# Kernel tuning notes

Hardware: AMD Instinct MI355X
Metric: run time of the kernel (lower is better)

Reference implementation:

```python
import jax, jax.numpy as jnp
import numpy as np

H = 64       # hidden size hard-coded in the module
NH = 4       # n_heads
S = 500      # stock_num
D = 10       # num_day
T = 40       # num_text (news per day)
FP = 3       # price features
FT = 512     # text embedding dim


def gru_scan(x, Wih, Whh, bih, bhh):
    """Single-sequence GRU (torch gate convention). x: (T, F) -> hidden states (T, H)."""
    gi = x @ Wih + bih  # (T, 3H) precompute input gates outside the scan

    def step(h, g):
        gh = h @ Whh + bhh
        r = jax.nn.sigmoid(g[:H] + gh[:H])
        z = jax.nn.sigmoid(g[H:2 * H] + gh[H:2 * H])
        n = jnp.tanh(g[2 * H:] + r * gh[2 * H:])
        h_new = (1.0 - z) * n + z * h
        return h_new, h_new

    h0 = jnp.zeros((H,), x.dtype)
    _, hs = jax.lax.scan(step, h0, gi)
    return hs


def attn_pool(hs, W, v):
    """Additive attention pooling over time. hs: (T, H) -> (H,)."""
    scores = jnp.tanh(hs @ W) @ v          # (T,)
    alpha = jax.nn.softmax(scores)
    return alpha @ hs


def _gru_params(key, fin, scale=0.08):
    k1, k2, k3, k4 = jax.random.split(key, 4)
    return (jax.random.normal(k1, (S, fin, 3 * H)) * scale,
            jax.random.normal(k2, (S, H, 3 * H)) * scale,
            jax.random.normal(k3, (S, 3 * H)) * scale,
            jax.random.normal(k4, (S, 3 * H)) * scale)


def _attn_params(key, scale=0.08):
    k1, k2 = jax.random.split(key)
    return (jax.random.normal(k1, (S, H, H)) * scale,
            jax.random.normal(k2, (S, H)) * scale)


def setup_inputs() -> dict:
    key = jax.random.key(0)
    ks = jax.random.split(key, 20)
    inp = {}
    inp['text_input'] = jax.random.normal(ks[0], (S, D, T, FT), dtype=jnp.float32)
    inp['price_input'] = jax.random.normal(ks[1], (S, D, FP), dtype=jnp.float32)
    inp['label'] = jax.random.randint(ks[2], (S,), 0, 2)
    inp['adj'] = jnp.ones((S, S), dtype=jnp.float32)
    inp['train'] = 0
    # per-stock stacked parameters
    (inp['Wih_p'], inp['Whh_p'], inp['bih_p'], inp['bhh_p']) = _gru_params(ks[3], FP)
    (inp['Wa_p'], inp['va_p']) = _attn_params(ks[4])
    (inp['Wih_t'], inp['Whh_t'], inp['bih_t'], inp['bhh_t']) = _gru_params(ks[5], FT)
    (inp['Wa_t'], inp['va_t']) = _attn_params(ks[6])
    (inp['Wih_s'], inp['Whh_s'], inp['bih_s'], inp['bhh_s']) = _gru_params(ks[7], H)
    (inp['Wa_s'], inp['va_s']) = _attn_params(ks[8])
    inp['Wb'] = jax.random.normal(ks[9], (S, H, H, H)) * 0.05   # Bilinear weight (out,in1,in2)
    inp['bb'] = jax.random.normal(ks[10], (S, H)) * 0.05
    inp['Wbl'] = jax.random.normal(ks[11], (S, H, 2)) * 0.08
    inp['bbl'] = jax.random.normal(ks[12], (S, 2)) * 0.08
    # shared cross-stock self-attention projections and final fc
    inp['Wq'] = jax.random.normal(ks[13], (H, H)) * 0.08
    inp['bq'] = jax.random.normal(ks[14], (H,)) * 0.08
    inp['Wk'] = jax.random.normal(ks[15], (H, H)) * 0.08
    inp['bk'] = jax.random.normal(ks[16], (H,)) * 0.08
    inp['Wf'] = jax.random.normal(ks[17], (H, 2)) * 0.08
    inp['bf'] = jax.random.normal(ks[18], (2,)) * 0.08
    return inp


def _forward(text_input, price_input, label,
             Wih_p, Whh_p, bih_p, bhh_p, Wa_p, va_p,
             Wih_t, Whh_t, bih_t, bhh_t, Wa_t, va_t,
             Wih_s, Whh_s, bih_s, bhh_s, Wa_s, va_s,
             Wb, bb, Wbl, bbl, Wq, bq, Wk, bk, Wf, bf):
    # ---- per-stock price encoder: GRU over days + attention pooling ----
    def enc_price(x, a, b, c, d, W, v):
        return attn_pool(gru_scan(x, a, b, c, d), W, v)
    x_price = jax.vmap(enc_price)(price_input, Wih_p, Whh_p, bih_p, bhh_p, Wa_p, va_p)  # (S, H)

    # ---- per-stock, per-day text encoder ----
    def enc_text_stock(xdays, a, b, c, d, W, v):
        return jax.vmap(lambda x: attn_pool(gru_scan(x, a, b, c, d), W, v))(xdays)  # (D, H)
    news = jax.vmap(enc_text_stock)(text_input, Wih_t, Whh_t, bih_t, bhh_t, Wa_t, va_t)  # (S, D, H)

    # ---- per-stock sequence encoder over days ----
    text_vec = jax.vmap(enc_price)(news, Wih_s, Whh_s, bih_s, bhh_s, Wa_s, va_s)  # (S, H)

    # ---- bilinear fusion: tanh(Bilinear(text, price)) ----
    combined = jnp.tanh(jnp.einsum('si,skij,sj->sk', text_vec, Wb, x_price) + bb)  # (S, H)

    # ---- per-stock blending head ----
    out_1 = jnp.tanh(jnp.einsum('si,sik->sk', combined, Wbl) + bbl)  # (S, 2)

    # ---- cross-stock multi-head self-attention (q,k projected, v identity) ----
    dh = H // NH
    q = (combined @ Wq + bq).reshape(S, NH, dh)
    k = (combined @ Wk + bk).reshape(S, NH, dh)
    v = combined.reshape(S, NH, dh)
    scores = jnp.einsum('shd,thd->hst', q, k) / (dh ** 0.5)
    attn = jax.nn.softmax(scores, axis=-1)
    attn_out = jnp.einsum('hst,thd->shd', attn, v).reshape(S, H)

    x = jax.nn.elu(attn_out @ Wf + bf)  # (S, 2)
    output = jax.nn.softmax(x + out_1, axis=1)
    # faithful to the original: CrossEntropyLoss applied to already-softmaxed output
    logp = jax.nn.log_softmax(output, axis=1)
    loss = -jnp.mean(logp[jnp.arange(S), label])
    return loss, output


def reference(text_input, price_input, label, adj, train,
              Wih_p, Whh_p, bih_p, bhh_p, Wa_p, va_p,
              Wih_t, Whh_t, bih_t, bhh_t, Wa_t, va_t,
              Wih_s, Whh_s, bih_s, bhh_s, Wa_s, va_s,
              Wb, bb, Wbl, bbl, Wq, bq, Wk, bk, Wf, bf):
    return _forward(text_input, price_input, label,
                    Wih_p, Whh_p, bih_p, bhh_p, Wa_p, va_p,
                    Wih_t, Whh_t, bih_t, bhh_t, Wa_t, va_t,
                    Wih_s, Whh_s, bih_s, bhh_s, Wa_s, va_s,
                    Wb, bb, Wbl, bbl, Wq, bq, Wk, bk, Wf, bf)
```

## Files before the change

kernel.cpp:

```cpp
#include <hip/hip_runtime.h>

#define Sn 500
#define Dn 10
#define Tn 40
#define FPn 3
#define FTn 512
#define Hn 64
#define G3 192
#define NHn 4

typedef __attribute__((ext_vector_type(8))) short bf8_t;
typedef __attribute__((ext_vector_type(4))) float f4_t;

__device__ __forceinline__ unsigned short f2bf(float f) {
    union { float f; unsigned int u; } v; v.f = f;
    unsigned int r = v.u + 0x7fffu + ((v.u >> 16) & 1u);
    return (unsigned short)(r >> 16);
}
__device__ __forceinline__ float bflo(unsigned int u) {
    union { unsigned int u; float f; } v; v.u = u << 16; return v.f;
}
__device__ __forceinline__ float bfhi(unsigned int u) {
    union { unsigned int u; float f; } v; v.u = u & 0xffff0000u; return v.f;
}
__device__ __forceinline__ unsigned int cvtpk(float lo, float hi) {
    unsigned int r;
    asm("v_cvt_pk_bf16_f32 %0, %1, %2" : "=v"(r) : "v"(lo), "v"(hi));
    return r;
}
__device__ __forceinline__ float sigmoidf_(float x) { return 1.f / (1.f + __expf(-x)); }
__device__ __forceinline__ float tanhf_(float x) {
    x = fminf(15.f, fmaxf(-15.f, x));
    float e = __expf(2.f * x);
    return (e - 1.f) / (e + 1.f);
}
__device__ __forceinline__ float dot8(uint4 wv, f4_t hA, f4_t hB) {
    return bflo(wv.x) * hA[0] + bfhi(wv.x) * hA[1]
         + bflo(wv.y) * hA[2] + bfhi(wv.y) * hA[3]
         + bflo(wv.z) * hB[0] + bfhi(wv.z) * hB[1]
         + bflo(wv.w) * hB[2] + bfhi(wv.w) * hB[3];
}
union bfu { bf8_t v; unsigned int u[4]; };

__global__ __launch_bounds__(256) void prep_fused(
    const float* __restrict__ Wih, unsigned short* __restrict__ wt,
    const float* __restrict__ price, const float* __restrict__ Wih_p,
    const float* __restrict__ Whh_p, const float* __restrict__ bih_p,
    const float* __restrict__ bhh_p, const float* __restrict__ Wa_p,
    const float* __restrict__ va_p, float* __restrict__ xprice)
{
    __shared__ float tile[64][65];
    __shared__ __align__(16) unsigned char smp[33160];

    const int bid = blockIdx.x, tid = threadIdx.x;

    if (bid < 12000) {
        const int s = bid / 24, tlo = bid % 24;
        const int kt = tlo / 3, ct = tlo % 3;
        const int k0 = kt * 64, c0 = ct * 64;

        const int c = tid & 63, r0 = tid >> 6;
        const float* src = Wih + ((size_t)s * FTn + k0) * G3 + c0 + c;
        #pragma unroll
        for (int i = 0; i < 16; ++i) {
            int r = i * 4 + r0;
            tile[c][r] = src[(size_t)r * G3];
        }
        __syncthreads();

        const int cl = tid >> 5, k2 = (tid & 31) * 2;
        unsigned int* wo = (unsigned int*)wt;
        const int kc = (k0 >> 3) + (k2 >> 3), e2 = (k2 & 7) >> 1;
        #pragma unroll
        for (int p = 0; p < 8; ++p) {
            int col = cl + p * 8;
            wo[(size_t)s * 49152 + ((size_t)kc * G3 + c0 + col) * 4 + e2] =
                cvtpk(tile[col][k2], tile[col][k2 + 1]);
        }
        return;
    }

    const int s = bid - 12000;
    if (tid >= 64) return;
    const int l = tid;
    unsigned char* whh2 = smp;
    unsigned char* wa2 = smp + 24576;
    float* hbuf = (float*)(smp + 32768);
    float* priceL = (float*)(smp + 33040);

    {
        const float* W3 = Whh_p + (size_t)s * Hn * G3;
        for (int r = 0; r < 192; ++r) {
            int e = l + r * 64, i = e / G3, j = e - i * G3;
            *(unsigned short*)(whh2 + j * 128 + ((2 * i) ^ ((j & 7) << 4))) = f2bf(W3[e]);
        }
        const float* A3 = Wa_p + (size_t)s * Hn * Hn;
        for (int r = 0; r < 64; ++r) {
            int e = l + r * 64, i = e >> 6, k = e & 63;
            *(unsigned short*)(wa2 + k * 128 + ((2 * i) ^ ((k & 7) << 4))) = f2bf(A3[e]);
        }
        if (l < 30) priceL[l] = price[(size_t)s * 30 + l];
        hbuf[l] = 0.f;
        if (l < 4) hbuf[64 + l] = 0.f;
    }
    __builtin_amdgcn_wave_barrier();
    {
        float wp[3][3];
        #pragma unroll
        for (int i = 0; i < 3; ++i)
            #pragma unroll
            for (int g = 0; g < 3; ++g)
                wp[i][g] = Wih_p[(size_t)s * 3 * G3 + i * G3 + g * 64 + l];
        const float bi0 = bih_p[(size_t)s * G3 + l];
        const float bi1 = bih_p[(size_t)s * G3 + 64 + l];
        const float bi2 = bih_p[(size_t)s * G3 + 128 + l];
        const float bh0 = bhh_p[(size_t)s * G3 + l];
        const float bh1 = bhh_p[(size_t)s * G3 + 64 + l];
        const float bh2 = bhh_p[(size_t)s * G3 + 128 + l];
        const float vak = va_p[(size_t)s * Hn + l];
        const int swl = (l & 7) << 4;
        float h3 = 0.f, m3 = -1e30f, den3 = 0.f, av3 = 0.f;
        for (int t = 0; t < Dn; ++t) {
            float x0 = priceL[t * 3], x1 = priceL[t * 3 + 1], x2 = priceL[t * 3 + 2];
            float gg0 = bi0 + x0 * wp[0][0] + x1 * wp[1][0] + x2 * wp[2][0];
            float gg1 = bi1 + x0 * wp[0][1] + x1 * wp[1][1] + x2 * wp[2][1];
            float gg2 = bi2 + x0 * wp[0][2] + x1 * wp[1][2] + x2 * wp[2][2];
            float gh0 = bh0, gh1 = bh1, gh2 = bh2;
            #pragma unroll
            for (int ic = 0; ic < 8; ++ic) {
                const int off = (ic * 16) ^ swl;
                f4_t hA = *(const f4_t*)&hbuf[ic * 8];
                f4_t hB = *(const f4_t*)&hbuf[ic * 8 + 4];
                uint4 w0 = *(const uint4*)(whh2 + l * 128 + off);
                uint4 w1 = *(const uint4*)(whh2 + (l + 64) * 128 + off);
                uint4 w2 = *(const uint4*)(whh2 + (l + 128) * 128 + off);
                gh0 += dot8(w0, hA, hB); gh1 += dot8(w1, hA, hB); gh2 += dot8(w2, hA, hB);
            }
            float r = sigmoidf_(gg0 + gh0);
            float z = sigmoidf_(gg1 + gh1);
            float n = tanhf_(gg2 + r * gh2);
            h3 = (1.f - z) * n + z * h3;
            __builtin_amdgcn_wave_barrier();
            hbuf[l] = h3;
            __builtin_amdgcn_wave_barrier();
            float sk = 0.f;
            #pragma unroll
            for (int ic = 0; ic < 8; ++ic) {
                const int off = (ic * 16) ^ swl;
                uint4 wv = *(const uint4*)(wa2 + l * 128 + off);
                f4_t hA = *(const f4_t*)&hbuf[ic * 8];
                f4_t hB = *(const f4_t*)&hbuf[ic * 8 + 4];
                sk += dot8(wv, hA, hB);
            }
            float term = tanhf_(sk) * vak;
            #pragma unroll
            for (int off = 32; off; off >>= 1) term += __shfl_xor(term, off);
            float mn = fmaxf(m3, term);
            float s0 = __expf(m3 - mn);
            float p = __expf(term - mn);
            den3 = den3 * s0 + p;
            av3 = av3 * s0 + p * h3;
            m3 = mn;
        }
        xprice[(size_t)s * Hn + l] = av3 / den3;
    }
}

__global__ __launch_bounds__(256) void main_fused(
    const float* __restrict__ text, const unsigned short* __restrict__ wt,
    const float* __restrict__ bih, float* __restrict__ gi2,
    const float* __restrict__ Wb, const float* __restrict__ xprice,
    float* __restrict__ u)
{
    __shared__ __align__(16) unsigned char sm[20480];

    const int id = blockIdx.x;
    const int grp = id / 9, sub = id - grp * 9;
    const int tid = threadIdx.x, w = tid >> 6, l = tid & 63;

    if (sub < 5) {
        const int s = grp, fi = sub;
        const int lr = l & 15, kg = l >> 4;
        unsigned short* Ab0 = (unsigned short*)sm;
        unsigned short* Ab1 = Ab0 + 5120;

        const float* xbase = text + ((size_t)s * 400 + fi * 80) * FTn;
        const unsigned short* wtb = wt + (size_t)s * 98304 + (size_t)(w * 48 + lr) * 8;

        const int c0 = tid, c1 = tid + 256, c2 = tid + 512;

        f4_t acc[5][3];
        #pragma unroll
        for (int a = 0; a < 5; a++)
            #pragma unroll
            for (int b = 0; b < 3; b++) acc[a][b] = (f4_t){0.f, 0.f, 0.f, 0.f};

        f4_t pa[3], pb[3];
        auto aload = [&](int kk) {
            #pragma unroll
            for (int q = 0; q < 3; ++q) {
                int c = tid + q * 256;
                if (q < 2 || tid < 128) {
                    int row = c >> 3, slot = c & 7;
                    const float* p = xbase + (size_t)row * FTn + kk * 64 + slot * 8;
                    pa[q] = *(const f4_t*)p; pb[q] = *(const f4_t*)(p + 4);
                }
            }
        };
        auto awrite = [&](unsigned short* buf) {
            #pragma unroll
            for (int q = 0; q < 3; ++q) {
                int c = tid + q * 256;
                if (q < 2 || tid < 128) {
                    int row = c >> 3, slot = c & 7;
                    uint4 uu = { cvtpk(pa[q][0], pa[q][1]), cvtpk(pa[q][2], pa[q][3]),
                                 cvtpk(pb[q][0], pb[q][1]), cvtpk(pb[q][2], pb[q][3]) };
                    *(uint4*)(buf + row * 64 + ((slot ^ (row & 7)) * 8)) = uu;
                }
            }
        };
        auto bload = [&](int kk, int ks, int nc) -> bf8_t {
            return *(const bf8_t*)(wtb + (size_t)((kk * 8 + ks * 4 + kg) * G3 + nc * 16) * 8);
        };
        auto afrag = [&](const unsigned short* buf, int mt, int ks) -> bf8_t {
            int row = mt * 16 + lr;
            int slot = (ks * 4 + kg) ^ (row & 7);
            return *(const bf8_t*)(buf + row * 64 + slot * 8);
        };

        bf8_t bc[2][3], bn[2][3];
        aload(0);
        #pragma unroll
        for (int ks = 0; ks < 2; ++ks)
            #pragma unroll
            for (int nc = 0; nc < 3; ++nc) bc[ks][nc] = bload(0, ks, nc);
        awrite(Ab0);
        __syncthreads();

        for (int kk = 0; kk < 8; ++kk) {
            unsigned short* cur = (kk & 1) ? Ab1 : Ab0;
            unsigned short* nxt = (kk & 1) ? Ab0 : Ab1;
            if (kk < 7) {
                aload(kk + 1);
                #pragma unroll
                for (int ks = 0; ks < 2; ++ks)
                    #pragma unroll
                    for (int nc = 0; nc < 3; ++nc) bn[ks][nc] = bload(kk + 1, ks, nc);
            }
            #pragma unroll
            for (int ks = 0; ks < 2; ++ks)
                #pragma unroll
                for (int mt = 0; mt < 5; ++mt) {
                    bf8_t af = afrag(cur, mt, ks);
                    acc[mt][0] = __builtin_amdgcn_mfma_f32_16x16x32_bf16(af, bc[ks][0], acc[mt][0], 0, 0, 0);
                    acc[mt][1] = __builtin_amdgcn_mfma_f32_16x16x32_bf16(af, bc[ks][1], acc[mt][1], 0, 0, 0);
                    acc[mt][2] = __builtin_amdgcn_mfma_f32_16x16x32_bf16(af, bc[ks][2], acc[mt][2], 0, 0, 0);
                }
            if (kk < 7) awrite(nxt);
            __syncthreads();
            #pragma unroll
            for (int ks = 0; ks < 2; ++ks)
                #pragma unroll
                for (int nc = 0; nc < 3; ++nc) bc[ks][nc] = bn[ks][nc];
        }

        const float* bihs = bih + (size_t)s * G3 + w * 48 + lr;
        #pragma unroll
        for (int nc = 0; nc < 3; ++nc) {
            const int col = w * 48 + nc * 16 + lr;
            const float bv = bihs[nc * 16];
            #pragma unroll
            for (int mt = 0; mt < 5; ++mt)
                #pragma unroll
                for (int rg = 0; rg < 4; ++rg) {
                    int r = mt * 16 + kg * 4 + rg;
                    int hi = (r >= 40);
                    int day = fi * 2 + hi;
                    int t = r - hi * 40;
                    gi2[((size_t)(s * 40 + t) * 10 + day) * 192 + col] = acc[mt][nc][rg] + bv;
                }
        }
    } else {
        const int s = grp, kq = sub - 5;
        float* uT = (float*)sm;
        const int j4 = (l & 15) * 4;
        f4_t xq = *(const f4_t*)&xprice[s * Hn + j4];

        const float* Wbs = Wb + (size_t)s * Hn * Hn * Hn;
        for (int g = 0; g < 64; ++g) {
            int P = kq * 1024 + w * 256 + g * 4 + (l >> 4);
            f4_t wv = *(const f4_t*)&Wbs[(size_t)P * Hn + j4];
            float dp = wv[0] * xq[0] + wv[1] * xq[1] + wv[2] * xq[2] + wv[3] * xq[3];
            dp += __shfl_xor(dp, 8);
            dp += __shfl_xor(dp, 4);
            dp += __shfl_xor(dp, 2);
            dp += __shfl_xor(dp, 1);
            if ((l & 15) == 0) { int k = P >> 6, i = P & 63; uT[i * 17 + (k - kq * 16)] = dp; }
        }
        __syncthreads();
        #pragma unroll
        for (int r = 0; r < 4; ++r) {
            int flat = tid + r * 256;
            int kr = flat >> 6, i = flat & 63;
            u[((size_t)s * 64 + kq * 16 + kr) * 64 + i] = uT[i * 17 + kr];
        }
    }
}

__global__ __launch_bounds__(64, 1) void gru_text_f(
    const float* __restrict__ gi2, const float* __restrict__ Whh,
    const float* __restrict__ bhh, const float* __restrict__ Wa,
    const float* __restrict__ va, float* __restrict__ news)
{
    __shared__ __align__(16) float hrow[16 * 68];
    __shared__ __align__(16) unsigned char waT[Hn * 128];

    const int s = blockIdx.x, l = threadIdx.x;
    const int lr = l & 15, lg = l >> 4;

    const float* Whhs = Whh + (size_t)s * Hn * G3;
    bfu bwhh[2][12];
    #pragma unroll
    for (int ks = 0; ks < 2; ++ks)
        #pragma unroll
        for (int nt = 0; nt < 12; ++nt) {
            const float* p = Whhs + (size_t)(ks * 32 + lg * 8) * G3 + nt * 16 + lr;
            float b0 = p[0], b1 = p[G3], b2 = p[2 * G3], b3 = p[3 * G3];
            float b4 = p[4 * G3], b5 = p[5 * G3], b6 = p[6 * G3], b7 = p[7 * G3];
            bwhh[ks][nt].u[0] = cvtpk(b0, b1); bwhh[ks][nt].u[1] = cvtpk(b2, b3);
            bwhh[ks][nt].u[2] = cvtpk(b4, b5); bwhh[ks][nt].u[3] = cvtpk(b6, b7);
        }
    float bhh_l[12];
    #pragma unroll
    for (int nt = 0; nt < 12; ++nt) bhh_l[nt] = bhh[(size_t)s * G3 + nt * 16 + lr];
    float va_l[4];
    #pragma unroll
    for (int nt = 0; nt < 4; ++nt) va_l[nt] = va[(size_t)s * Hn + nt * 16 + lr];

    {
        const float* Was = Wa + (size_t)s * Hn * Hn;
        for (int r = 0; r < 64; ++r) {
            int e = l + r * 64, i = e >> 6, k = e & 63;
            *(unsigned short*)(waT + k * 128 + ((2 * i) ^ ((k & 7) << 4))) = f2bf(Was[e]);
        }
        #pragma unroll
        for (int r = 0; r < 17; ++r) hrow[l + r * 64] = 0.f;
    }
    __builtin_amdgcn_wave_barrier();

    int dayoff[4];
    #pragma unroll
    for (int rr = 0; rr < 4; ++rr) {
        int d = lg * 4 + rr; if (d > 9) d = 9;
        dayoff[rr] = d * 192 + lr;
    }
    const float* gbase = gi2 + (size_t)s * 40 * 1920;

    float val[48], valn[48];
    #pragma unroll
    for (int j = 0; j < 48; ++j) val[j] = gbase[dayoff[j & 3] + (j >> 2) * 16];

    bf8_t a0f, a1f;
    {   bfu z0; z0.u[0] = 0; z0.u[1] = 0; z0.u[2] = 0; z0.u[3] = 0; a0f = z0.v; a1f = z0.v; }

    float h[4][4], accv[4][4], den[4], m[4];
    #pragma unroll
    for (int nt = 0; nt < 4; ++nt)
        #pragma unroll
        for (int rr = 0; rr < 4; ++rr) { h[nt][rr] = 0.f; accv[nt][rr] = 0.f; }
    #pragma unroll
    for (int rr = 0; rr < 4; ++rr) { den[rr] = 0.f; m[rr] = -1e30f; }

    for (int t = 0; t < Tn; ++t) {
        f4_t acc[12];
        #pragma unroll
        for (int nt = 0; nt < 12; ++nt)
            acc[nt] = (f4_t){bhh_l[nt], bhh_l[nt], bhh_l[nt], bhh_l[nt]};
        __builtin_amdgcn_s_setprio(1);
        #pragma unroll
        for (int nt = 0; nt < 12; ++nt) {
            acc[nt] = __builtin_amdgcn_mfma_f32_16x16x32_bf16(a0f, bwhh[0][nt].v, acc[nt], 0, 0, 0);
            acc[nt] = __builtin_amdgcn_mfma_f32_16x16x32_bf16(a1f, bwhh[1][nt].v, acc[nt], 0, 0, 0);
        }
        __builtin_amdgcn_s_setprio(0);
        {
            const int tn = (t < Tn - 1) ? t + 1 : t;
            const float* gb = gbase + (size_t)tn * 1920;
            #pragma unroll
            for (int j = 0; j < 48; ++j) valn[j] = gb[dayoff[j & 3] + (j >> 2) * 16];
        }
        #pragma unroll
        for (int nt = 0; nt < 4; ++nt)
            #pragma unroll
            for (int rr = 0; rr < 4; ++rr) {
                float r = sigmoidf_(val[nt * 4 + rr] + acc[nt][rr]);
                float z = sigmoidf_(val[(nt + 4) * 4 + rr] + acc[nt + 4][rr]);
                float n = tanhf_(val[(nt + 8) * 4 + rr] + r * acc[nt + 8][rr]);
                h[nt][rr] = (1.f - z) * n + z * h[nt][rr];
            }
        __builtin_amdgcn_wave_barrier();
        #pragma unroll
        for (int rr = 0; rr < 4; ++rr) {
            int day = lg * 4 + rr;
            if (day < Dn) {
                #pragma unroll
                for (int nt = 0; nt < 4; ++nt) hrow[day * 68 + nt * 16 + lr] = h[nt][rr];
            }
        }
        __builtin_amdgcn_wave_barrier();
        {
            const float* hp = hrow + lr * 68 + lg * 8;
            f4_t x0 = *(const f4_t*)hp,        x1 = *(const f4_t*)(hp + 4);
            f4_t y0 = *(const f4_t*)(hp + 32), y1 = *(const f4_t*)(hp + 36);
            bfu t0, t1;
            t0.u[0] = cvtpk(x0[0], x0[1]); t0.u[1] = cvtpk(x0[2], x0[3]);
            t0.u[2] = cvtpk(x1[0], x1[1]); t0.u[3] = cvtpk(x1[2], x1[3]);
            t1.u[0] = cvtpk(y0[0], y0[1]); t1.u[1] = cvtpk(y0[2], y0[3]);
            t1.u[2] = cvtpk(y1[0], y1[1]); t1.u[3] = cvtpk(y1[2], y1[3]);
            a0f = t0.v; a1f = t1.v;
        }
        f4_t sc[4];
        #pragma unroll
        for (int nt = 0; nt < 4; ++nt) sc[nt] = (f4_t){0.f, 0.f, 0.f, 0.f};
        __builtin_amdgcn_s_setprio(1);
        #pragma unroll
        for (int ks = 0; ks < 2; ++ks) {
            bf8_t av = ks ? a1f : a0f;
            #pragma unroll
            for (int nt = 0; nt < 4; ++nt) {
                bf8_t bwv = *(const bf8_t*)(waT + (nt * 16 + lr) * 128
                                            + ((ks * 64 + lg * 16) ^ ((lr & 7) << 4)));
                sc[nt] = __builtin_amdgcn_mfma_f32_16x16x32_bf16(av, bwv, sc[nt], 0, 0, 0);
            }
        }
        __builtin_amdgcn_s_setprio(0);
        float pr[4];
        #pragma unroll
        for (int rr = 0; rr < 4; ++rr) {
            pr[rr] = tanhf_(sc[0][rr]) * va_l[0] + tanhf_(sc[1][rr]) * va_l[1]
                   + tanhf_(sc[2][rr]) * va_l[2] + tanhf_(sc[3][rr]) * va_l[3];
            pr[rr] += __shfl_xor(pr[rr], 1);
            pr[rr] += __shfl_xor(pr[rr], 2);
            pr[rr] += __shfl_xor(pr[rr], 4);
            pr[rr] += __shfl_xor(pr[rr], 8);
        }
        #pragma unroll
        for (int rr = 0; rr < 4; ++rr) {
            float mn = fmaxf(m[rr], pr[rr]);
            float s0 = __expf(m[rr] - mn);
            float p = __expf(pr[rr] - mn);
            den[rr] = den[rr] * s0 + p;
            #pragma unroll
            for (int nt = 0; nt < 4; ++nt)
                accv[nt][rr] = accv[nt][rr] * s0 + p * h[nt][rr];
            m[rr] = mn;
        }
        #pragma unroll
        for (int j = 0; j < 48; ++j) val[j] = valn[j];
    }
    #pragma unroll
    for (int rr = 0; rr < 4; ++rr) {
        int day = lg * 4 + rr;
        if (day < Dn) {
            float inv = 1.f / den[rr];
            #pragma unroll
            for (int nt = 0; nt < 4; ++nt)
                news[((size_t)s * Dn + day) * Hn + nt * 16 + lr] = accv[nt][rr] * inv;
        }
    }
}

__global__ __launch_bounds__(64, 1) void day_finish(
    const float* __restrict__ news,
    const float* __restrict__ Wih_s, const float* __restrict__ Whh_s,
    const float* __restrict__ bih_s, const float* __restrict__ bhh_s,
    const float* __restrict__ Wa_s, const float* __restrict__ va_s,
    const float* __restrict__ u, const float* __restrict__ bb,
    const float* __restrict__ Wq, const float* __restrict__ bq,
    const float* __restrict__ Wk, const float* __restrict__ bk,
    const float* __restrict__ Wbl, const float* __restrict__ bbl,
    float* __restrict__ combined, float* __restrict__ qg,
    float* __restrict__ kg, float* __restrict__ out1)
{
    __shared__ __align__(16) unsigned char sm[60928];
    unsigned char* whh2 = sm;
    unsigned char* wih2 = sm + 24576;
    unsigned char* wa2 = sm + 49152;
    float* newsL = (float*)(sm + 57600);
    float* hbuf  = (float*)(sm + 60320);

    const int s = blockIdx.x, l = threadIdx.x;
    float tvv;

    {
        const float* W2 = Whh_s + (size_t)s * Hn * G3;
        const float* X2 = Wih_s + (size_t)s * Hn * G3;
        for (int r = 0; r < 192; ++r) {
            int e = l + r * 64, i = e / G3, j = e - i * G3;
            int off = j * 128 + ((2 * i) ^ ((j & 7) << 4));
            *(unsigned short*)(whh2 + off) = f2bf(W2[e]);
            *(unsigned short*)(wih2 + off) = f2bf(X2[e]);
        }
        const float* A2 = Wa_s + (size_t)s * Hn * Hn;
        for (int r = 0; r < 64; ++r) {
            int e = l + r * 64, i = e >> 6, k = e & 63;
            *(unsigned short*)(wa2 + k * 128 + ((2 * i) ^ ((k & 7) << 4))) = f2bf(A2[e]);
        }
        #pragma unroll
        for (int d = 0; d < Dn; ++d) newsL[d * 68 + l] = news[((size_t)s * Dn + d) * Hn + l];
        hbuf[l] = 0.f;
        if (l < 4) hbuf[64 + l] = 0.f;
    }
    __builtin_amdgcn_wave_barrier();
    {
        const float bi0 = bih_s[(size_t)s * G3 + l];
        const float bi1 = bih_s[(size_t)s * G3 + 64 + l];
        const float bi2 = bih_s[(size_t)s * G3 + 128 + l];
        const float bh0 = bhh_s[(size_t)s * G3 + l];
        const float bh1 = bhh_s[(size_t)s * G3 + 64 + l];
        const float bh2 = bhh_s[(size_t)s * G3 + 128 + l];
        const float vak = va_s[(size_t)s * Hn + l];
        const int swl = (l & 7) << 4;
        float h2 = 0.f, m2 = -1e30f, den2 = 0.f, av2 = 0.f;
        for (int t = 0; t < Dn; ++t) {
            float gh0 = bh0, gh1 = bh1, gh2 = bh2;
            float gg0 = bi0, gg1 = bi1, gg2 = bi2;
            #pragma unroll
            for (int ic = 0; ic < 8; ++ic) {
                const int off = (ic * 16) ^ swl;
                f4_t hA = *(const f4_t*)&hbuf[ic * 8];
                f4_t hB = *(const f4_t*)&hbuf[ic * 8 + 4];
                f4_t nA = *(const f4_t*)&newsL[t * 68 + ic * 8];
                f4_t nB = *(const f4_t*)&newsL[t * 68 + ic * 8 + 4];
                uint4 w0 = *(const uint4*)(whh2 + l * 128 + off);
                uint4 w1 = *(const uint4*)(whh2 + (l + 64) * 128 + off);
                uint4 w2 = *(const uint4*)(whh2 + (l + 128) * 128 + off);
                uint4 x0 = *(const uint4*)(wih2 + l * 128 + off);
                uint4 x1 = *(const uint4*)(wih2 + (l + 64) * 128 + off);
                uint4 x2 = *(const uint4*)(wih2 + (l + 128) * 128 + off);
                gh0 += dot8(w0, hA, hB); gh1 += dot8(w1, hA, hB); gh2 += dot8(w2, hA, hB);
                gg0 += dot8(x0, nA, nB); gg1 += dot8(x1, nA, nB); gg2 += dot8(x2, nA, nB);
            }
            float r = sigmoidf_(gg0 + gh0);
            float z = sigmoidf_(gg1 + gh1);
            float n = tanhf_(gg2 + r * gh2);
            h2 = (1.f - z) * n + z * h2;
            __builtin_amdgcn_wave_barrier();
            hbuf[l] = h2;
            __builtin_amdgcn_wave_barrier();
            float sk = 0.f;
            #pragma unroll
            for (int ic = 0; ic < 8; ++ic) {
                const int off = (ic * 16) ^ swl;
                uint4 wv = *(const uint4*)(wa2 + l * 128 + off);
                f4_t hA = *(const f4_t*)&hbuf[ic * 8];
                f4_t hB = *(const f4_t*)&hbuf[ic * 8 + 4];
                sk += dot8(wv, hA, hB);
            }
            float term = tanhf_(sk) * vak;
            #pragma unroll
            for (int off = 32; off; off >>= 1) term += __shfl_xor(term, off);
            float mn = fmaxf(m2, term);
            float s0 = __expf(m2 - mn);
            float p = __expf(term - mn);
            den2 = den2 * s0 + p;
            av2 = av2 * s0 + p * h2;
            m2 = mn;
        }
        tvv = av2 / den2;
    }
    __builtin_amdgcn_wave_barrier();

    float* uL = (float*)sm;
    float* tvL = (float*)(sm + 16640);
    float* cl  = (float*)(sm + 16960);
    tvL[l] = tvv;
    const float* ub = u + (size_t)s * 4096;
    #pragma unroll 8
    for (int i = 0; i < 64; ++i) uL[i * 65 + l] = ub[i * 64 + l];
    __builtin_amdgcn_wave_barrier();
    {
        float a = bb[s * Hn + l];
        #pragma unroll 8
        for (int i = 0; i < 64; ++i) a += tvL[i] * uL[l * 65 + i];
        float c = tanhf_(a);
        cl[l] = c;
        combined[s * Hn + l] = c;
    }
    __builtin_amdgcn_wave_barrier();
    {
        float aq = bq[l], ak = bk[l];
        for (int i = 0; i < Hn; i++) {
            float ci = cl[i];
            aq += ci * Wq[i * Hn + l];
            ak += ci * Wk[i * Hn + l];
        }
        qg[s * Hn + l] = aq; kg[s * Hn + l] = ak;
        if (l < 2) {
            float a = bbl[s * 2 + l];
            for (int i = 0; i < Hn; i++) a += cl[i] * Wbl[(size_t)s * Hn * 2 + i * 2 + l];
            out1[s * 2 + l] = tanhf_(a);
        }
    }
}

__global__ __launch_bounds__(256) void mhsa(
    const float* __restrict__ qg, const float* __restrict__ kg,
    const float* __restrict__ combined, const float* __restrict__ Wf,
    const float* __restrict__ bfp, const float* __restrict__ out1,
    float* __restrict__ dout)
{
    __shared__ __align__(16) float ql[Hn];
    __shared__ float sl[NHn][Sn];
    __shared__ float hsum[NHn];
    __shared__ float ao[Hn];
    __shared__ float red2[8];
    __shared__ float red3[4][Hn];

    const int sq = blockIdx.x, tid = threadIdx.x;
    if (tid < Hn) ql[tid] = qg[sq * Hn + tid];
    __syncthreads();

    for (int id = tid; id < Sn * NHn; id += 256) {
        int t = id >> 2, h = id & 3;
        const float* kp = &kg[t * Hn + h * 16];
        float a = 0.f;
        #pragma unroll
        for (int x = 0; x < 16; x += 4) {
            f4_t kv = *(const f4_t*)&kp[x];
            f4_t qv = *(const f4_t*)&ql[h * 16 + x];
            a += kv[0] * qv[0] + kv[1] * qv[1] + kv[2] * qv[2] + kv[3] * qv[3];
        }
        sl[h][t] = a * 0.25f;
    }
    __syncthreads();
    for (int h = 0; h < NHn; ++h) {
        float m = -1e30f;
        for (int t = tid; t < Sn; t += 256) m = fmaxf(m, sl[h][t]);
        for (int o = 32; o; o >>= 1) m = fmaxf(m, __shfl_xor(m, o));
        if ((tid & 63) == 0) red2[tid >> 6] = m;
        __syncthreads();
        m = fmaxf(fmaxf(red2[0], red2[1]), fmaxf(red2[2], red2[3]));
        float ps = 0.f;
        for (int t = tid; t < Sn; t += 256) { float p = __expf(sl[h][t] - m); sl[h][t] = p; ps += p; }
        for (int o = 32; o; o >>= 1) ps += __shfl_xor(ps, o);
        if ((tid & 63) == 0) red2[4 + (tid >> 6)] = ps;
        __syncthreads();
        if (tid == 0) hsum[h] = red2[4] + red2[5] + red2[6] + red2[7];
        __syncthreads();
    }
    {
        const int q = tid >> 6, j = tid & 63, h = j >> 4;
        float a = 0.f;
        for (int t = q * 125; t < q * 125 + 125; ++t) a += sl[h][t] * combined[t * Hn + j];
        red3[q][j] = a;
    }
    __syncthreads();
    if (tid < Hn)
        ao[tid] = (red3[0][tid] + red3[1][tid] + red3[2][tid] + red3[3][tid]) / hsum[tid >> 4];
    __syncthreads();
    if (tid == 0) {
        float l0 = bfp[0], l1 = bfp[1];
        for (int j = 0; j < Hn; j++) { float v = ao[j]; l0 += v * Wf[j * 2]; l1 += v * Wf[j * 2 + 1]; }
        l0 = l0 > 0.f ? l0 : __expf(l0) - 1.f;
        l1 = l1 > 0.f ? l1 : __expf(l1) - 1.f;
        l0 += out1[sq * 2]; l1 += out1[sq * 2 + 1];
        float m = fmaxf(l0, l1);
        float e0 = __expf(l0 - m), e1 = __expf(l1 - m);
        float inv = 1.f / (e0 + e1);
        dout[1 + sq * 2] = e0 * inv;
        dout[2 + sq * 2] = e1 * inv;
    }
}

__global__ __launch_bounds__(512) void loss_k(float* __restrict__ dout,
                                              const int* __restrict__ label)
{
    __shared__ float red[512];
    const int tid = threadIdx.x;
    float a = 0.f;
    if (tid < Sn) {
        float p0 = dout[1 + 2 * tid], p1 = dout[2 + 2 * tid];
        float m = fmaxf(p0, p1);
        float lse = m + __logf(__expf(p0 - m) + __expf(p1 - m));
        float pl = label[tid] ? p1 : p0;
        a = -(pl - lse);
    }
    red[tid] = a;
    __syncthreads();
    for (int o = 256; o; o >>= 1) {
        if (tid < o) red[tid] += red[tid + o];
        __syncthreads();
    }
    if (tid == 0) dout[0] = red[0] / (float)Sn;
}

extern "C" void kernel_launch(void* const* d_in, const int* in_sizes, int n_in,
                              void* d_out, int out_size, void* d_ws, size_t ws_size,
                              hipStream_t stream)
{
    const float* text  = (const float*)d_in[0];
    const float* price = (const float*)d_in[1];
    const int*   label = (const int*)  d_in[2];
    const float* Wih_p = (const float*)d_in[5];
    const float* Whh_p = (const float*)d_in[6];
    const float* bih_p = (const float*)d_in[7];
    const float* bhh_p = (const float*)d_in[8];
    const float* Wa_p  = (const float*)d_in[9];
    const float* va_p  = (const float*)d_in[10];
    const float* Wih_t = (const float*)d_in[11];
    const float* Whh_t = (const float*)d_in[12];
    const float* bih_t = (const float*)d_in[13];
    const float* bhh_t = (const float*)d_in[14];
    const float* Wa_t  = (const float*)d_in[15];
    const float* va_t  = (const float*)d_in[16];
    const float* Wih_s = (const float*)d_in[17];
    const float* Whh_s = (const float*)d_in[18];
    const float* bih_s = (const float*)d_in[19];
    const float* bhh_s = (const float*)d_in[20];
    const float* Wa_s  = (const float*)d_in[21];
    const float* va_s  = (const float*)d_in[22];
    const float* Wb    = (const float*)d_in[23];
    const float* bb    = (const float*)d_in[24];
    const float* Wbl   = (const float*)d_in[25];
    const float* bbl   = (const float*)d_in[26];
    const float* Wq    = (const float*)d_in[27];
    const float* bq    = (const float*)d_in[28];
    const float* Wk    = (const float*)d_in[29];
    const float* bk    = (const float*)d_in[30];
    const float* Wf    = (const float*)d_in[31];
    const float* bf_   = (const float*)d_in[32];

    float* ws = (float*)d_ws;
    float* news     = ws;
    float* xprice   = ws + 320000;
    float* combined = ws + 384000;
    float* qg       = ws + 416000;
    float* kg       = ws + 448000;
    float* out1     = ws + 480000;
    float* u        = ws + 481000;
    float* gi2      = ws + 2529000;
    unsigned short* wt = (unsigned short*)(ws + 40929000);
    float* dout = (float*)d_out;

    prep_fused<<<12500, 256, 0, stream>>>(Wih_t, wt,
                                          price, Wih_p, Whh_p, bih_p, bhh_p, Wa_p, va_p,
                                          xprice);
    main_fused<<<4500, 256, 0, stream>>>(text, wt, bih_t, gi2, Wb, xprice, u);
    gru_text_f<<<Sn, 64, 0, stream>>>(gi2, Whh_t, bhh_t, Wa_t, va_t, news);
    day_finish<<<Sn, 64, 0, stream>>>(news,
                                      Wih_s, Whh_s, bih_s, bhh_s, Wa_s, va_s,
                                      u, bb, Wq, bq, Wk, bk, Wbl, bbl,
                                      combined, qg, kg, out1);
    mhsa<<<Sn, 256, 0, stream>>>(qg, kg, combined, Wf, bf_, out1, dout);
    loss_k<<<1, 512, 0, stream>>>(dout, label);
}
```

Baseline: 638.2 us.

## Fuse Wih transpose into GEMM B-loads, split Wb work finer, swizzle blocks by XCD

Removes the separate pre-transpose/bf16 conversion pass of the text GRU input weights. The GEMM now loads fp32 Wih directly with strided per-element reads and converts to bf16 in registers. The price GRU becomes its own small kernel. The Wb projection is split into 8 sub-blocks per stock instead of 4, giving 13 sub-blocks per stock, and block IDs are remapped so a stock's blocks land on the same XCD for L2 locality. This saves a full write/read round trip of the converted weights, at the cost of uncoalesced strided B loads repeated by the 5 M-blocks per stock.

```diff
diff --git a/kernel.cpp b/kernel.cpp
--- a/kernel.cpp
+++ b/kernel.cpp
@@ -42,52 +42,19 @@
 }
 union bfu { bf8_t v; unsigned int u[4]; };
 
-__global__ __launch_bounds__(256) void prep_fused(
-    const float* __restrict__ Wih, unsigned short* __restrict__ wt,
+__global__ __launch_bounds__(64, 1) void price_gru(
     const float* __restrict__ price, const float* __restrict__ Wih_p,
     const float* __restrict__ Whh_p, const float* __restrict__ bih_p,
     const float* __restrict__ bhh_p, const float* __restrict__ Wa_p,
     const float* __restrict__ va_p, float* __restrict__ xprice)
 {
-    __shared__ float tile[64][65];
     __shared__ __align__(16) unsigned char smp[33160];
-
-    const int bid = blockIdx.x, tid = threadIdx.x;
-
-    if (bid < 12000) {
-        const int s = bid / 24, tlo = bid % 24;
-        const int kt = tlo / 3, ct = tlo % 3;
-        const int k0 = kt * 64, c0 = ct * 64;
-
-        const int c = tid & 63, r0 = tid >> 6;
-        const float* src = Wih + ((size_t)s * FTn + k0) * G3 + c0 + c;
-        #pragma unroll
-        for (int i = 0; i < 16; ++i) {
-            int r = i * 4 + r0;
-            tile[c][r] = src[(size_t)r * G3];
-        }
-        __syncthreads();
-
-        const int cl = tid >> 5, k2 = (tid & 31) * 2;
-        unsigned int* wo = (unsigned int*)wt;
-        const int kc = (k0 >> 3) + (k2 >> 3), e2 = (k2 & 7) >> 1;
-        #pragma unroll
-        for (int p = 0; p < 8; ++p) {
-            int col = cl + p * 8;
-            wo[(size_t)s * 49152 + ((size_t)kc * G3 + c0 + col) * 4 + e2] =
-                cvtpk(tile[col][k2], tile[col][k2 + 1]);
-        }
-        return;
-    }
-
-    const int s = bid - 12000;
-    if (tid >= 64) return;
-    const int l = tid;
     unsigned char* whh2 = smp;
     unsigned char* wa2 = smp + 24576;
     float* hbuf = (float*)(smp + 32768);
     float* priceL = (float*)(smp + 33040);
 
+    const int s = blockIdx.x, l = threadIdx.x;
     {
         const float* W3 = Whh_p + (size_t)s * Hn * G3;
         for (int r = 0; r < 192; ++r) {
@@ -166,16 +133,18 @@
     }
 }
 
-__global__ __launch_bounds__(256) void main_fused(
-    const float* __restrict__ text, const unsigned short* __restrict__ wt,
+__global__ __launch_bounds__(256) void mega_fused(
+    const float* __restrict__ text, const float* __restrict__ Wih,
     const float* __restrict__ bih, float* __restrict__ gi2,
     const float* __restrict__ Wb, const float* __restrict__ xprice,
     float* __restrict__ u)
 {
     __shared__ __align__(16) unsigned char sm[20480];
 
-    const int id = blockIdx.x;
-    const int grp = id / 9, sub = id - grp * 9;
+    const int bid = blockIdx.x;
+    const int xcd = bid & 7, ix = bid >> 3;
+    const int swz = (xcd < 4 ? xcd * 813 : 3252 + (xcd - 4) * 812) + ix;
+    const int grp = swz / 13, sub = swz - grp * 13;
     const int tid = threadIdx.x, w = tid >> 6, l = tid & 63;
 
     if (sub < 5) {
@@ -185,9 +154,7 @@
         unsigned short* Ab1 = Ab0 + 5120;
 
         const float* xbase = text + ((size_t)s * 400 + fi * 80) * FTn;
-        const unsigned short* wtb = wt + (size_t)s * 98304 + (size_t)(w * 48 + lr) * 8;
-
-        const int c0 = tid, c1 = tid + 256, c2 = tid + 512;
+        const float* Wihs = Wih + (size_t)s * FTn * G3 + w * 48 + lr;
 
         f4_t acc[5][3];
         #pragma unroll
@@ -220,7 +187,13 @@
             }
         };
         auto bload = [&](int kk, int ks, int nc) -> bf8_t {
-            return *(const bf8_t*)(wtb + (size_t)((kk * 8 + ks * 4 + kg) * G3 + nc * 16) * 8);
+            const float* bp = Wihs + (size_t)(kk * 64 + ks * 32 + kg * 8) * G3 + nc * 16;
+            float b0 = bp[0], b1 = bp[G3], b2 = bp[2 * G3], b3 = bp[3 * G3];
+            float b4 = bp[4 * G3], b5 = bp[5 * G3], b6 = bp[6 * G3], b7 = bp[7 * G3];
+            bfu t;
+            t.u[0] = cvtpk(b0, b1); t.u[1] = cvtpk(b2, b3);
+            t.u[2] = cvtpk(b4, b5); t.u[3] = cvtpk(b6, b7);
+            return t.v;
         };
         auto afrag = [&](const unsigned short* buf, int mt, int ks) -> bf8_t {
             int row = mt * 16 + lr;
@@ -287,22 +260,22 @@
         f4_t xq = *(const f4_t*)&xprice[s * Hn + j4];
 
         const float* Wbs = Wb + (size_t)s * Hn * Hn * Hn;
-        for (int g = 0; g < 64; ++g) {
-            int P = kq * 1024 + w * 256 + g * 4 + (l >> 4);
+        for (int g = 0; g < 32; ++g) {
+            int P = kq * 512 + g * 16 + w * 4 + (l >> 4);
             f4_t wv = *(const f4_t*)&Wbs[(size_t)P * Hn + j4];
             float dp = wv[0] * xq[0] + wv[1] * xq[1] + wv[2] * xq[2] + wv[3] * xq[3];
             dp += __shfl_xor(dp, 8);
             dp += __shfl_xor(dp, 4);
             dp += __shfl_xor(dp, 2);
             dp += __shfl_xor(dp, 1);
-            if ((l & 15) == 0) { int k = P >> 6, i = P & 63; uT[i * 17 + (k - kq * 16)] = dp; }
+            if ((l & 15) == 0) { int k = P >> 6, i = P & 63; uT[i * 9 + (k - kq * 8)] = dp; }
         }
         __syncthreads();
         #pragma unroll
-        for (int r = 0; r < 4; ++r) {
+        for (int r = 0; r < 2; ++r) {
             int flat = tid + r * 256;
-            int kr = flat >> 6, i = flat & 63;
-            u[((size_t)s * 64 + kq * 16 + kr) * 64 + i] = uT[i * 17 + kr];
+            int kL = flat >> 6, i = flat & 63;
+            u[((size_t)s * 64 + kq * 8 + kL) * 64 + i] = uT[i * 9 + kL];
         }
     }
 }
@@ -740,13 +713,10 @@
     float* out1     = ws + 480000;
     float* u        = ws + 481000;
     float* gi2      = ws + 2529000;
-    unsigned short* wt = (unsigned short*)(ws + 40929000);
     float* dout = (float*)d_out;
 
-    prep_fused<<<12500, 256, 0, stream>>>(Wih_t, wt,
-                                          price, Wih_p, Whh_p, bih_p, bhh_p, Wa_p, va_p,
-                                          xprice);
-    main_fused<<<4500, 256, 0, stream>>>(text, wt, bih_t, gi2, Wb, xprice, u);
+    price_gru<<<Sn, 64, 0, stream>>>(price, Wih_p, Whh_p, bih_p, bhh_p, Wa_p, va_p, xprice);
+    mega_fused<<<6500, 256, 0, stream>>>(text, Wih_t, bih_t, gi2, Wb, xprice, u);
     gru_text_f<<<Sn, 64, 0, stream>>>(gi2, Whh_t, bhh_t, Wa_t, va_t, news);
     day_finish<<<Sn, 64, 0, stream>>>(news,
                                       Wih_s, Whh_s, bih_s, bhh_s, Wa_s, va_s,
```

After: 622.9 us. -2.4%, faster.
